# Kernel tuning notes

Measured on AMD Instinct MI355X. Metric: run time of the kernel, lower is better.

## Reference

```python
import jax, jax.numpy as jnp
import numpy as np

B, S, D = 1, 2048, 2048
H, KV = 32, 8
HD = D // H          # 64
R = H // KV          # 4 (GQA repeat factor)
ROPE_BASE = 10000.0


def setup_inputs() -> dict:
    key = jax.random.key(0)
    ks = jax.random.split(key, 5)
    x = jax.random.normal(ks[0], (B, S, D), jnp.float32)
    # Real rotary frequencies as (cos, sin) pairs: [S, HD//2, 2]
    inv_freq = 1.0 / (ROPE_BASE ** (np.arange(0, HD, 2, dtype=np.float64) / HD))
    ang = np.outer(np.arange(S, dtype=np.float64), inv_freq)
    freqs_cis = jnp.asarray(np.stack([np.cos(ang), np.sin(ang)], axis=-1), jnp.float32)
    std = 0.02
    wq = jax.random.normal(ks[1], (H * HD, D), jnp.float32) * std
    wk = jax.random.normal(ks[2], (KV * HD, D), jnp.float32) * std
    wv = jax.random.normal(ks[3], (KV * HD, D), jnp.float32) * std
    wo = jax.random.normal(ks[4], (D, H * HD), jnp.float32) * std
    return {"x": x, "freqs_cis": freqs_cis, "wq": wq, "wk": wk, "wv": wv, "wo": wo}


def _apply_rope(x, cos, sin):
    # x: [b, s, h, hd]; cos/sin: [s, hd//2]. Complex multiply on interleaved pairs.
    xr = x.reshape(*x.shape[:-1], HD // 2, 2)
    x0, x1 = xr[..., 0], xr[..., 1]
    c = cos[None, :, None, :]
    s = sin[None, :, None, :]
    o0 = x0 * c - x1 * s
    o1 = x0 * s + x1 * c
    return jnp.stack([o0, o1], axis=-1).reshape(x.shape)


def reference(x, freqs_cis, wq, wk, wv, wo):
    b, s, _ = x.shape
    q = (x @ wq.T).reshape(b, s, H, HD)
    k = (x @ wk.T).reshape(b, s, KV, HD)
    v = (x @ wv.T).reshape(b, s, KV, HD)
    cos, sin = freqs_cis[..., 0], freqs_cis[..., 1]
    q = _apply_rope(q, cos, sin)
    k = _apply_rope(k, cos, sin)
    # GQA: group q heads instead of repeat_interleave on k/v.
    # repeat_interleave maps kv-head g -> q heads [g*R, (g+1)*R), matching this reshape.
    qg = q.reshape(b, s, KV, R, HD)
    scale = 1.0 / np.sqrt(HD)
    scores = jnp.einsum('bsgrd,btgd->bgrst', qg, k) * scale  # [b, KV, R, s, t]
    causal = jnp.tril(jnp.ones((s, s), dtype=bool))
    scores = jnp.where(causal, scores, jnp.float32(-1e9))
    attn = jax.nn.softmax(scores.astype(jnp.float32), axis=-1).astype(q.dtype)
    out = jnp.einsum('bgrst,btgd->bsgrd', attn, v).reshape(b, s, H * HD)
    return out @ wo.T
```

## Files before the change

### kernel.cpp

```cpp
#include <hip/hip_runtime.h>

typedef unsigned short u16;
typedef unsigned int u32;
typedef __bf16 bf16x8 __attribute__((ext_vector_type(8)));
typedef unsigned short ushort8 __attribute__((ext_vector_type(8)));
typedef float floatx4 __attribute__((ext_vector_type(4)));

#define S_LEN 2048
#define NH 32
#define NKV 8
#define HD_ 64
#define LDQ 3072

__device__ __forceinline__ u16 f2bf(float f) {
  unsigned u = __builtin_bit_cast(unsigned, f);
  u += 0x7FFF + ((u >> 16) & 1);
  return (u16)(u >> 16);
}
__device__ __forceinline__ float bf2f(u16 h) {
  unsigned u = ((unsigned)h) << 16;
  return __builtin_bit_cast(float, u);
}
__device__ __forceinline__ bf16x8 ld8(const u16* p) {
  return __builtin_bit_cast(bf16x8, *(const ushort8*)p);
}
__device__ __forceinline__ floatx4 mfma16(bf16x8 a, bf16x8 b, floatx4 c) {
  return __builtin_amdgcn_mfma_f32_16x16x32_bf16(a, b, c, 0, 0, 0);
}
__device__ __forceinline__ u32 pk2bf(float a, float b) {
  u32 ua = __builtin_bit_cast(u32, a) + 0x8000u;
  u32 ub = __builtin_bit_cast(u32, b) + 0x8000u;
  return __builtin_amdgcn_perm(ub, ua, 0x07060302);
}
__device__ __forceinline__ ushort8 pack8(float4 a, float4 b) {
  union { u32 w[4]; ushort8 v; } u;
  u.w[0] = pk2bf(a.x, a.y); u.w[1] = pk2bf(a.z, a.w);
  u.w[2] = pk2bf(b.x, b.y); u.w[3] = pk2bf(b.z, b.w);
  return u.v;
}

template <int A_F32, int OUT_BF16>
__global__ __launch_bounds__(256) void gemm_pipe(
    const void* __restrict__ Avoid, const float* __restrict__ B0,
    const float* __restrict__ B1, const float* __restrict__ B2,
    int seg1, int seg2, void* __restrict__ C, int N, int K, int lda) {
  __shared__ __align__(16) u16 As[128 * 64];
  __shared__ __align__(16) u16 Bs[64 * 64];
  const int tid = threadIdx.x;
  const int wave = tid >> 6, lane = tid & 63;
  const int quad = lane >> 4, l16 = lane & 15;
  const int bm = blockIdx.y * 128, bn = blockIdx.x * 64;
  const int wr = (wave >> 1) * 64, wc = (wave & 1) * 32;
  const int crow = tid >> 3, col8 = tid & 7;

  const float* Af = (const float*)Avoid;
  const u16*   Ab = (const u16*)Avoid;

  const float* bptr[2];
#pragma unroll
  for (int j = 0; j < 2; j++) {
    int r = bn + crow + j * 32;
    bptr[j] = (r < seg1) ? B0 + (size_t)r * K
            : (r < seg2) ? B1 + (size_t)(r - seg1) * K
                         : B2 + (size_t)(r - seg2) * K;
  }
  size_t aoff[4];
#pragma unroll
  for (int j = 0; j < 4; j++) aoff[j] = (size_t)(bm + crow + j * 32) * lda + col8 * 8;

  float4 a4[4][2]; ushort8 a8[4]; float4 b4[2][2];
  auto load_tiles = [&](int k0) {
    if constexpr (A_F32) {
#pragma unroll
      for (int j = 0; j < 4; j++) {
        a4[j][0] = *(const float4*)(Af + aoff[j] + k0);
        a4[j][1] = *(const float4*)(Af + aoff[j] + k0 + 4);
      }
    } else {
#pragma unroll
      for (int j = 0; j < 4; j++) a8[j] = *(const ushort8*)(Ab + aoff[j] + k0);
    }
#pragma unroll
    for (int j = 0; j < 2; j++) {
      b4[j][0] = *(const float4*)(bptr[j] + k0 + col8 * 8);
      b4[j][1] = *(const float4*)(bptr[j] + k0 + col8 * 8 + 4);
    }
  };

  floatx4 acc[4][2] = {};
  load_tiles(0);
  for (int k0 = 0; k0 < K; k0 += 64) {
#pragma unroll
    for (int j = 0; j < 4; j++) {
      const int row = crow + j * 32;
      ushort8 v;
      if constexpr (A_F32) v = pack8(a4[j][0], a4[j][1]);
      else                 v = a8[j];
      *(ushort8*)&As[row * 64 + ((col8 ^ (row & 7)) * 8)] = v;
    }
#pragma unroll
    for (int j = 0; j < 2; j++) {
      const int row = crow + j * 32;
      *(ushort8*)&Bs[row * 64 + ((col8 ^ (row & 7)) * 8)] = pack8(b4[j][0], b4[j][1]);
    }
    __syncthreads();
    if (k0 + 64 < K) load_tiles(k0 + 64);
#pragma unroll
    for (int kh = 0; kh < 2; kh++) {
      bf16x8 af[4], bfr[2];
#pragma unroll
      for (int mi = 0; mi < 4; mi++) {
        const int row = wr + mi * 16 + l16;
        af[mi] = ld8(&As[row * 64 + (((kh * 4 + quad) ^ (row & 7)) * 8)]);
      }
#pragma unroll
      for (int ni = 0; ni < 2; ni++) {
        const int row = wc + ni * 16 + l16;
        bfr[ni] = ld8(&Bs[row * 64 + (((kh * 4 + quad) ^ (row & 7)) * 8)]);
      }
#pragma unroll
      for (int mi = 0; mi < 4; mi++)
#pragma unroll
        for (int ni = 0; ni < 2; ni++)
          acc[mi][ni] = mfma16(af[mi], bfr[ni], acc[mi][ni]);
    }
    __syncthreads();
  }

#pragma unroll
  for (int mi = 0; mi < 4; mi++)
#pragma unroll
    for (int ni = 0; ni < 2; ni++)
#pragma unroll
      for (int r = 0; r < 4; r++) {
        const int row = bm + wr + mi * 16 + quad * 4 + r;
        const int col = bn + wc + ni * 16 + l16;
        if (OUT_BF16) ((u16*)C)[(size_t)row * N + col] = f2bf(acc[mi][ni][r]);
        else          ((float*)C)[(size_t)row * N + col] = acc[mi][ni][r];
      }
}

__global__ void rope_kernel(u16* __restrict__ qk, const float* __restrict__ fc, int h_bits,
                            int row_stride, float scale) {
  int idx = blockIdx.x * blockDim.x + threadIdx.x;
  int d = idx & 31;
  int t = idx >> 5;
  int hh = t & ((1 << h_bits) - 1);
  int s = t >> h_bits;
  float c  = fc[s * 64 + d * 2];
  float sn = fc[s * 64 + d * 2 + 1];
  size_t base = (size_t)s * row_stride + hh * 64 + d * 2;
  float x0 = bf2f(qk[base]), x1 = bf2f(qk[base + 1]);
  qk[base]     = f2bf((x0 * c - x1 * sn) * scale);
  qk[base + 1] = f2bf((x0 * sn + x1 * c) * scale);
}

__global__ void transpose_v(const u16* __restrict__ qkv, u16* __restrict__ vT) {
  int idx = blockIdx.x * blockDim.x + threadIdx.x;
  int s = idx & (S_LEN - 1);
  int t = idx >> 11;
  vT[idx] = qkv[(size_t)s * LDQ + 2560 + t];
}

__global__ __launch_bounds__(256) void attn_kernel(const u16* qkv, const u16* __restrict__ vT,
                                                   u16* __restrict__ o) {
  __shared__ __align__(16) u16 Ks[64 * 72];
  __shared__ __align__(16) u16 Vs[64 * 72];
  __shared__ __align__(16) u16 pS[4][16 * 72];
  const int h = blockIdx.x;
  const int qt = (h & 1) ? (31 - (int)blockIdx.y) : (int)blockIdx.y;
  const int g = h >> 2;
  const int tid = threadIdx.x;
  const int wave = tid >> 6, lane = tid & 63;
  const int quad = lane >> 4, l16 = lane & 15;
  const int qglob = qt * 64 + wave * 16 + l16;

  const size_t qoff = (size_t)qglob * LDQ + h * HD_;
  bf16x8 qf0 = ld8(qkv + qoff + quad * 8);
  bf16x8 qf1 = ld8(qkv + qoff + 32 + quad * 8);

  const ushort8 ones_u = {0x3F80, 0x3F80, 0x3F80, 0x3F80, 0x3F80, 0x3F80, 0x3F80, 0x3F80};
  const bf16x8 onesA = __builtin_bit_cast(bf16x8, ones_u);

  const int r0 = tid >> 3,         o0 = (tid & 7) * 8;
  const int r1 = (tid + 256) >> 3, o1 = o0;
  const u16* ksrc = qkv + 2048 + g * HD_;
  const u16* vsrc = vT + (size_t)g * HD_ * S_LEN;

  ushort8 kp0 = *(const ushort8*)(ksrc + (size_t)r0 * LDQ + o0);
  ushort8 kp1 = *(const ushort8*)(ksrc + (size_t)r1 * LDQ + o1);
  ushort8 vp0 = *(const ushort8*)(vsrc + (size_t)r0 * S_LEN + o0);
  ushort8 vp1 = *(const ushort8*)(vsrc + (size_t)r1 * S_LEN + o1);

  floatx4 Ofrag[4] = {};
  floatx4 lacc = {};
  u16* myP = &pS[wave][0];

  for (int kt = 0; kt <= qt; kt++) {
    const int kbase = kt * 64;
    *(ushort8*)&Ks[r0 * 72 + o0] = kp0;
    *(ushort8*)&Ks[r1 * 72 + o1] = kp1;
    *(ushort8*)&Vs[r0 * 72 + o0] = vp0;
    *(ushort8*)&Vs[r1 * 72 + o1] = vp1;
    __syncthreads();
    if (kt < qt) {
      const int nb = kbase + 64;
      kp0 = *(const ushort8*)(ksrc + (size_t)(nb + r0) * LDQ + o0);
      kp1 = *(const ushort8*)(ksrc + (size_t)(nb + r1) * LDQ + o1);
      vp0 = *(const ushort8*)(vsrc + (size_t)r0 * S_LEN + nb + o0);
      vp1 = *(const ushort8*)(vsrc + (size_t)r1 * S_LEN + nb + o1);
    }
    floatx4 sf[4];
#pragma unroll
    for (int sub = 0; sub < 4; sub++) {
      const u16* kb = &Ks[(sub * 16 + l16) * 72];
      floatx4 s = {};
      s = mfma16(ld8(kb + quad * 8), qf0, s);
      s = mfma16(ld8(kb + 32 + quad * 8), qf1, s);
      sf[sub] = s;
    }
    if (kt == qt) {
#pragma unroll
      for (int sub = 0; sub < 4; sub++)
#pragma unroll
        for (int r = 0; r < 4; r++)
          if (kbase + sub * 16 + quad * 4 + r > qglob) sf[sub][r] = -INFINITY;
    }
    u32 pk[4][2];
#pragma unroll
    for (int sub = 0; sub < 4; sub++)
#pragma unroll
      for (int w = 0; w < 2; w++) {
        float p0 = __builtin_amdgcn_exp2f(sf[sub][2 * w]);
        float p1 = __builtin_amdgcn_exp2f(sf[sub][2 * w + 1]);
        pk[sub][w] = pk2bf(p0, p1);
      }
    bf16x8 vf[4][2];
#pragma unroll
    for (int nt = 0; nt < 4; nt++) {
      const u16* vb = &Vs[(nt * 16 + l16) * 72 + quad * 8];
      vf[nt][0] = ld8(vb);
      vf[nt][1] = ld8(vb + 32);
    }
#pragma unroll
    for (int sub = 0; sub < 4; sub++)
#pragma unroll
      for (int w = 0; w < 2; w++)
        *(u32*)&myP[l16 * 72 + sub * 16 + quad * 4 + 2 * w] = pk[sub][w];
    asm volatile("s_waitcnt lgkmcnt(0)" ::: "memory");
    bf16x8 pf0 = ld8(&myP[l16 * 72 + quad * 8]);
    bf16x8 pf1 = ld8(&myP[l16 * 72 + 32 + quad * 8]);
#pragma unroll
    for (int nt = 0; nt < 4; nt++) {
      Ofrag[nt] = mfma16(vf[nt][0], pf0, Ofrag[nt]);
      Ofrag[nt] = mfma16(vf[nt][1], pf1, Ofrag[nt]);
    }
    lacc = mfma16(onesA, pf0, lacc);
    lacc = mfma16(onesA, pf1, lacc);
    __syncthreads();
  }

  const float inv = 1.0f / lacc[0];
  const size_t ooff = (size_t)qglob * 2048 + h * HD_;
#pragma unroll
  for (int nt = 0; nt < 4; nt++)
#pragma unroll
    for (int r = 0; r < 4; r++) {
      int hd = nt * 16 + quad * 4 + r;
      o[ooff + hd] = f2bf(Ofrag[nt][r] * inv);
    }
}

extern "C" void kernel_launch(void* const* d_in, const int* in_sizes, int n_in,
                              void* d_out, int out_size, void* d_ws, size_t ws_size,
                              hipStream_t stream) {
  const float* x  = (const float*)d_in[0];
  const float* fc = (const float*)d_in[1];
  const float* wq = (const float*)d_in[2];
  const float* wk = (const float*)d_in[3];
  const float* wv = (const float*)d_in[4];
  const float* wo = (const float*)d_in[5];
  float* out = (float*)d_out;

  char* ws = (char*)d_ws;
  const size_t MB = 1024 * 1024;
  u16* qkv = (u16*)(ws);
  u16* vTb = (u16*)(ws + 12 * MB);
  u16* ob  = (u16*)(ws + 14 * MB);
  (void)ws_size; (void)n_in; (void)in_sizes; (void)out_size;

  const int BIG = 1 << 30;
  gemm_pipe<1, 1><<<dim3(48, 16), 256, 0, stream>>>(
      x, wq, wk, wv, 2048, 2560, qkv, LDQ, 2048, 2048);
  rope_kernel<<<8192, 256, 0, stream>>>(qkv, fc, 5, LDQ, 0.18033688f);
  rope_kernel<<<2048, 256, 0, stream>>>(qkv + 2048, fc, 3, LDQ, 1.0f);
  transpose_v<<<4096, 256, 0, stream>>>(qkv, vTb);
  attn_kernel<<<dim3(NH, S_LEN / 64), 256, 0, stream>>>(qkv, vTb, ob);
  gemm_pipe<0, 0><<<dim3(32, 16), 256, 0, stream>>>(
      ob, wo, wo, wo, BIG, BIG, out, 2048, 2048, 2048);
}
```

Measured before the change: 245.6 us.

## Pre-convert inputs and weights to bf16 and use double-buffered GEMM tiles

Adds a separate fp32-to-bf16 conversion kernel for x and all weight matrices, so the GEMMs read bf16 operands directly instead of converting inside the main loop. The GEMM kernel is rewritten with double-buffered shared memory, so only one barrier is needed per k-step and global loads overlap the MFMA work. The QKV projection now uses 128x128 tiles. The change adds extra launches and extra memory traffic for the conversions, and it uses the output buffer and a reused workspace region as scratch, which relies on those buffers not being live at the same time.

```diff
diff --git a/kernel.cpp b/kernel.cpp
--- a/kernel.cpp
+++ b/kernel.cpp
@@ -32,111 +32,98 @@
   u32 ub = __builtin_bit_cast(u32, b) + 0x8000u;
   return __builtin_amdgcn_perm(ub, ua, 0x07060302);
 }
-__device__ __forceinline__ ushort8 pack8(float4 a, float4 b) {
-  union { u32 w[4]; ushort8 v; } u;
-  u.w[0] = pk2bf(a.x, a.y); u.w[1] = pk2bf(a.z, a.w);
-  u.w[2] = pk2bf(b.x, b.y); u.w[3] = pk2bf(b.z, b.w);
-  return u.v;
-}
-
-template <int A_F32, int OUT_BF16>
-__global__ __launch_bounds__(256) void gemm_pipe(
-    const void* __restrict__ Avoid, const float* __restrict__ B0,
-    const float* __restrict__ B1, const float* __restrict__ B2,
-    int seg1, int seg2, void* __restrict__ C, int N, int K, int lda) {
-  __shared__ __align__(16) u16 As[128 * 64];
-  __shared__ __align__(16) u16 Bs[64 * 64];
+
+__global__ void cvt_kernel(const float* __restrict__ in, u16* __restrict__ out, int n4) {
+  int i = blockIdx.x * blockDim.x + threadIdx.x;
+  if (i >= n4) return;
+  float4 v = ((const float4*)in)[i];
+  ((ushort4*)out)[i] = make_ushort4(f2bf(v.x), f2bf(v.y), f2bf(v.z), f2bf(v.w));
+}
+
+template <int TM, int TN, int OUT_BF16>
+__global__ __launch_bounds__(256) void gemm_db(
+    const u16* __restrict__ A, const u16* __restrict__ B, void* __restrict__ C,
+    int ldc, int K, int lda) {
+  __shared__ __align__(16) u16 As[2][TM * 64];
+  __shared__ __align__(16) u16 Bs[2][TN * 64];
   const int tid = threadIdx.x;
   const int wave = tid >> 6, lane = tid & 63;
   const int quad = lane >> 4, l16 = lane & 15;
-  const int bm = blockIdx.y * 128, bn = blockIdx.x * 64;
-  const int wr = (wave >> 1) * 64, wc = (wave & 1) * 32;
+  const int bm = blockIdx.y * TM, bn = blockIdx.x * TN;
+  const int wr = (wave >> 1) * (TM / 2), wc = (wave & 1) * (TN / 2);
+  constexpr int MI = TM / 32, NI = TN / 32;
   const int crow = tid >> 3, col8 = tid & 7;
 
-  const float* Af = (const float*)Avoid;
-  const u16*   Ab = (const u16*)Avoid;
-
-  const float* bptr[2];
-#pragma unroll
-  for (int j = 0; j < 2; j++) {
-    int r = bn + crow + j * 32;
-    bptr[j] = (r < seg1) ? B0 + (size_t)r * K
-            : (r < seg2) ? B1 + (size_t)(r - seg1) * K
-                         : B2 + (size_t)(r - seg2) * K;
+  size_t aoff[MI], boff[NI];
+#pragma unroll
+  for (int j = 0; j < MI; j++) aoff[j] = (size_t)(bm + crow + j * 32) * lda + col8 * 8;
+#pragma unroll
+  for (int j = 0; j < NI; j++) boff[j] = (size_t)(bn + crow + j * 32) * K + col8 * 8;
+
+  ushort8 a8[MI], b8[NI];
+  auto load_tiles = [&](int k0) {
+#pragma unroll
+    for (int j = 0; j < MI; j++) a8[j] = *(const ushort8*)(A + aoff[j] + k0);
+#pragma unroll
+    for (int j = 0; j < NI; j++) b8[j] = *(const ushort8*)(B + boff[j] + k0);
+  };
+  auto write_tiles = [&](int p) {
+#pragma unroll
+    for (int j = 0; j < MI; j++) {
+      const int row = crow + j * 32;
+      *(ushort8*)&As[p][row * 64 + ((col8 ^ (row & 7)) * 8)] = a8[j];
+    }
+#pragma unroll
+    for (int j = 0; j < NI; j++) {
+      const int row = crow + j * 32;
+      *(ushort8*)&Bs[p][row * 64 + ((col8 ^ (row & 7)) * 8)] = b8[j];
+    }
+  };
+
+  floatx4 acc[MI][NI] = {};
+  load_tiles(0);
+  write_tiles(0);
+  __syncthreads();
+  int p = 0;
+  for (int k0 = 0; k0 < K; k0 += 64) {
+    const bool more = (k0 + 64 < K);
+    if (more) load_tiles(k0 + 64);
+#pragma unroll
+    for (int kh = 0; kh < 2; kh++) {
+      bf16x8 af[MI], bfr[NI];
+#pragma unroll
+      for (int mi = 0; mi < MI; mi++) {
+        const int row = wr + mi * 16 + l16;
+        af[mi] = ld8(&As[p][row * 64 + (((kh * 4 + quad) ^ (row & 7)) * 8)]);
+      }
+#pragma unroll
+      for (int ni = 0; ni < NI; ni++) {
+        const int row = wc + ni * 16 + l16;
+        bfr[ni] = ld8(&Bs[p][row * 64 + (((kh * 4 + quad) ^ (row & 7)) * 8)]);
+      }
+#pragma unroll
+      for (int mi = 0; mi < MI; mi++)
+#pragma unroll
+        for (int ni = 0; ni < NI; ni++)
+          acc[mi][ni] = mfma16(af[mi], bfr[ni], acc[mi][ni]);
+    }
+    if (more) {
+      write_tiles(p ^ 1);
+      __syncthreads();
+      p ^= 1;
+    }
   }
-  size_t aoff[4];
-#pragma unroll
-  for (int j = 0; j < 4; j++) aoff[j] = (size_t)(bm + crow + j * 32) * lda + col8 * 8;
-
-  float4 a4[4][2]; ushort8 a8[4]; float4 b4[2][2];
-  auto load_tiles = [&](int k0) {
-    if constexpr (A_F32) {
-#pragma unroll
-      for (int j = 0; j < 4; j++) {
-        a4[j][0] = *(const float4*)(Af + aoff[j] + k0);
-        a4[j][1] = *(const float4*)(Af + aoff[j] + k0 + 4);
-      }
-    } else {
-#pragma unroll
-      for (int j = 0; j < 4; j++) a8[j] = *(const ushort8*)(Ab + aoff[j] + k0);
-    }
-#pragma unroll
-    for (int j = 0; j < 2; j++) {
-      b4[j][0] = *(const float4*)(bptr[j] + k0 + col8 * 8);
-      b4[j][1] = *(const float4*)(bptr[j] + k0 + col8 * 8 + 4);
-    }
-  };
-
-  floatx4 acc[4][2] = {};
-  load_tiles(0);
-  for (int k0 = 0; k0 < K; k0 += 64) {
-#pragma unroll
-    for (int j = 0; j < 4; j++) {
-      const int row = crow + j * 32;
-      ushort8 v;
-      if constexpr (A_F32) v = pack8(a4[j][0], a4[j][1]);
-      else                 v = a8[j];
-      *(ushort8*)&As[row * 64 + ((col8 ^ (row & 7)) * 8)] = v;
-    }
-#pragma unroll
-    for (int j = 0; j < 2; j++) {
-      const int row = crow + j * 32;
-      *(ushort8*)&Bs[row * 64 + ((col8 ^ (row & 7)) * 8)] = pack8(b4[j][0], b4[j][1]);
-    }
-    __syncthreads();
-    if (k0 + 64 < K) load_tiles(k0 + 64);
-#pragma unroll
-    for (int kh = 0; kh < 2; kh++) {
-      bf16x8 af[4], bfr[2];
-#pragma unroll
-      for (int mi = 0; mi < 4; mi++) {
-        const int row = wr + mi * 16 + l16;
-        af[mi] = ld8(&As[row * 64 + (((kh * 4 + quad) ^ (row & 7)) * 8)]);
-      }
-#pragma unroll
-      for (int ni = 0; ni < 2; ni++) {
-        const int row = wc + ni * 16 + l16;
-        bfr[ni] = ld8(&Bs[row * 64 + (((kh * 4 + quad) ^ (row & 7)) * 8)]);
-      }
-#pragma unroll
-      for (int mi = 0; mi < 4; mi++)
-#pragma unroll
-        for (int ni = 0; ni < 2; ni++)
-          acc[mi][ni] = mfma16(af[mi], bfr[ni], acc[mi][ni]);
-    }
-    __syncthreads();
-  }
-
-#pragma unroll
-  for (int mi = 0; mi < 4; mi++)
-#pragma unroll
-    for (int ni = 0; ni < 2; ni++)
+
+#pragma unroll
+  for (int mi = 0; mi < MI; mi++)
+#pragma unroll
+    for (int ni = 0; ni < NI; ni++)
 #pragma unroll
       for (int r = 0; r < 4; r++) {
         const int row = bm + wr + mi * 16 + quad * 4 + r;
         const int col = bn + wc + ni * 16 + l16;
-        if (OUT_BF16) ((u16*)C)[(size_t)row * N + col] = f2bf(acc[mi][ni][r]);
-        else          ((float*)C)[(size_t)row * N + col] = acc[mi][ni][r];
+        if (OUT_BF16) ((u16*)C)[(size_t)row * ldc + col] = f2bf(acc[mi][ni][r]);
+        else          ((float*)C)[(size_t)row * ldc + col] = acc[mi][ni][r];
       }
 }
 
@@ -285,17 +272,22 @@
   char* ws = (char*)d_ws;
   const size_t MB = 1024 * 1024;
   u16* qkv = (u16*)(ws);
+  u16* wb  = (u16*)(ws + 12 * MB);
   u16* vTb = (u16*)(ws + 12 * MB);
-  u16* ob  = (u16*)(ws + 14 * MB);
+  u16* wob = (u16*)(ws + 14 * MB);
+  u16* ob  = (u16*)(ws + 22 * MB);
+  u16* xb  = (u16*)d_out;
   (void)ws_size; (void)n_in; (void)in_sizes; (void)out_size;
 
-  const int BIG = 1 << 30;
-  gemm_pipe<1, 1><<<dim3(48, 16), 256, 0, stream>>>(
-      x, wq, wk, wv, 2048, 2560, qkv, LDQ, 2048, 2048);
+  cvt_kernel<<<4096, 256, 0, stream>>>(x,  xb, 1048576);
+  cvt_kernel<<<4096, 256, 0, stream>>>(wq, wb, 1048576);
+  cvt_kernel<<<1024, 256, 0, stream>>>(wk, wb + (size_t)2048 * 2048, 262144);
+  cvt_kernel<<<1024, 256, 0, stream>>>(wv, wb + (size_t)2560 * 2048, 262144);
+  gemm_db<128, 128, 1><<<dim3(24, 16), 256, 0, stream>>>(xb, wb, qkv, LDQ, 2048, 2048);
+  cvt_kernel<<<4096, 256, 0, stream>>>(wo, wob, 1048576);
   rope_kernel<<<8192, 256, 0, stream>>>(qkv, fc, 5, LDQ, 0.18033688f);
   rope_kernel<<<2048, 256, 0, stream>>>(qkv + 2048, fc, 3, LDQ, 1.0f);
   transpose_v<<<4096, 256, 0, stream>>>(qkv, vTb);
   attn_kernel<<<dim3(NH, S_LEN / 64), 256, 0, stream>>>(qkv, vTb, ob);
-  gemm_pipe<0, 0><<<dim3(32, 16), 256, 0, stream>>>(
-      ob, wo, wo, wo, BIG, BIG, out, 2048, 2048, 2048);
-}
+  gemm_db<128, 64, 0><<<dim3(32, 16), 256, 0, stream>>>(ob, wob, out, 2048, 2048, 2048);
+}
```

Result: no change. 243.3 us (-0.9%).
